# Kernel optimization log

Measured on AMD Instinct MI355X. Metric: run time of the kernel, lower is better.

Reference implementation:

```python
import jax, jax.numpy as jnp
import numpy as np

B, S, D = 4, 2048, 1024
H = 4 * D          # expert hidden dim
E_SPEC = 4         # num specific experts
E_SHR = 2          # num shared experts
TOP_K = 2


def setup_inputs() -> dict:
    key = jax.random.key(0)
    ks = jax.random.split(key, 16)
    s = 0.02
    return {
        "x": jax.random.normal(ks[0], (B, S, D), jnp.float32),
        # specific experts (stacked over expert axis)
        "spec_w1": jax.random.normal(ks[1], (E_SPEC, D, H), jnp.float32) * s,
        "spec_b1": jnp.zeros((E_SPEC, H), jnp.float32),
        "spec_w2": jax.random.normal(ks[2], (E_SPEC, H, D), jnp.float32) * s,
        "spec_b2": jnp.zeros((E_SPEC, D), jnp.float32),
        "spec_rw": jax.random.normal(ks[3], (D, E_SPEC), jnp.float32) * s,
        "spec_rb": jnp.zeros((E_SPEC,), jnp.float32),
        # shared experts
        "shr_w1": jax.random.normal(ks[4], (E_SHR, D, H), jnp.float32) * s,
        "shr_b1": jnp.zeros((E_SHR, H), jnp.float32),
        "shr_w2": jax.random.normal(ks[5], (E_SHR, H, D), jnp.float32) * s,
        "shr_b2": jnp.zeros((E_SHR, D), jnp.float32),
        "shr_rw": jax.random.normal(ks[6], (D, E_SHR), jnp.float32) * s,
        "shr_rb": jnp.zeros((E_SHR,), jnp.float32),
    }


def _expert_mlp(xf, w1, b1, w2, b2):
    # xf: [T, D]; w1: [E, D, H]; w2: [E, H, D] -> [E, T, D]
    h = jax.nn.gelu(jnp.einsum("td,edh->eth", xf, w1) + b1[:, None, :],
                    approximate=False)
    return jnp.einsum("eth,ehd->etd", h, w2) + b2[:, None, :]


def reference(x, spec_w1, spec_b1, spec_w2, spec_b2, spec_rw, spec_rb,
              shr_w1, shr_b1, shr_w2, shr_b2, shr_rw, shr_rb):
    b, s, d = x.shape
    xf = x.reshape(-1, d)                      # [T, D]
    T = xf.shape[0]

    # --- specific (top-k) routing ---
    spec_probs = jax.nn.softmax(xf @ spec_rw + spec_rb, axis=-1)   # [T, E]
    topk_probs, topk_idx = jax.lax.top_k(spec_probs, TOP_K)        # [T, K]

    # aux load-balancing loss
    counts = jnp.zeros((E_SPEC,), jnp.float32).at[topk_idx.reshape(-1)].add(1.0)
    fraction = counts / (T * TOP_K)
    aux_loss = E_SPEC * jnp.sum(fraction * spec_probs.mean(axis=0))

    # gate[t, e] = sum_k topk_probs[t,k] * 1[topk_idx[t,k]==e]
    gate = jnp.sum(jax.nn.one_hot(topk_idx, E_SPEC, dtype=xf.dtype)
                   * topk_probs[..., None], axis=1)                # [T, E]

    spec_out_e = _expert_mlp(xf, spec_w1, spec_b1, spec_w2, spec_b2)  # [E, T, D]
    specific_out = jnp.einsum("te,etd->td", gate, spec_out_e)

    # --- shared (dense) experts ---
    shr_probs = jax.nn.softmax(xf @ shr_rw + shr_rb, axis=-1)      # [T, E_shr]
    shr_out_e = _expert_mlp(xf, shr_w1, shr_b1, shr_w2, shr_b2)    # [E_shr, T, D]
    shared_out = jnp.einsum("te,etd->td", shr_probs, shr_out_e)

    final = (specific_out + shared_out).reshape(b, s, d)
    return final, aux_loss
```

## Files before the change

kernel.cpp:

```cpp
#include <hip/hip_runtime.h>
#include <hip/hip_bf16.h>

#define T_TOK 8192
#define DDIM 1024
#define HDIM 4096

typedef __bf16 bf16;
typedef bf16 bf16x8 __attribute__((ext_vector_type(8)));
typedef float f32x4 __attribute__((ext_vector_type(4)));

#define ASM_VMCNT(n) asm volatile("s_waitcnt vmcnt(" #n ")" ::: "memory")
#define MFMA16(a, b, c) __builtin_amdgcn_mfma_f32_16x16x32_bf16((a), (b), (c), 0, 0, 0)
#define G8_BAR __builtin_amdgcn_s_barrier()
#define G8_WAIT                                            \
  asm volatile("s_waitcnt lgkmcnt(0)" ::: "memory");       \
  __builtin_amdgcn_sched_barrier(0)

__device__ __forceinline__ void gl_lds16(const void* g, void* l) {
  __builtin_amdgcn_global_load_lds(
      (const __attribute__((address_space(1))) unsigned int*)g,
      (__attribute__((address_space(3))) unsigned int*)l, 16, 0, 0);
}

__device__ __forceinline__ float gelu_f(float v) {
  const float x = v * 0.7071067811865475f;
  const float ax = fabsf(x);
  const float t = 1.0f / fmaf(0.3275911f, ax, 1.0f);
  float p = fmaf(1.061405429f, t, -1.453152027f);
  p = fmaf(p, t, 1.421413741f);
  p = fmaf(p, t, -0.284496736f);
  p = fmaf(p, t, 0.254829592f);
  p = p * t;
  const float e = __expf(-ax * ax);
  const float er = fmaf(-p, e, 1.0f);
  const float erfx = (x >= 0.0f) ? er : -er;
  return 0.5f * v * (1.0f + erfx);
}

__global__ __launch_bounds__(256) void conv_router(
    const float* __restrict__ x, bf16* __restrict__ xb,
    const float* __restrict__ srw, const float* __restrict__ srb,
    const float* __restrict__ hrw, const float* __restrict__ hrb,
    float* __restrict__ gate, float4* __restrict__ probs4,
    int* __restrict__ top2) {
  const int lane = threadIdx.x & 63;
  const int w = threadIdx.x >> 6;
  const int t = blockIdx.x * 4 + w;

  const float* xr = x + (size_t)t * DDIM;
  bf16* xbr = xb + (size_t)t * DDIM;
  float p0 = 0, p1 = 0, p2 = 0, p3 = 0, p4 = 0, p5 = 0;
#pragma unroll
  for (int c = 0; c < 4; ++c) {
    const int d = c * 256 + lane * 4;
    const float4 xv = *(const float4*)(xr + d);
    bf16 ov[4] = {(bf16)xv.x, (bf16)xv.y, (bf16)xv.z, (bf16)xv.w};
    *(float2*)(xbr + d) = *(float2*)ov;
    const float xa[4] = {xv.x, xv.y, xv.z, xv.w};
#pragma unroll
    for (int j = 0; j < 4; ++j) {
      const float xd = xa[j];
      const float4 r4 = *(const float4*)(srw + (size_t)(d + j) * 4);
      p0 += xd * r4.x; p1 += xd * r4.y; p2 += xd * r4.z; p3 += xd * r4.w;
      const float2 r2 = *(const float2*)(hrw + (size_t)(d + j) * 2);
      p4 += xd * r2.x; p5 += xd * r2.y;
    }
  }
#pragma unroll
  for (int off = 32; off >= 1; off >>= 1) {
    p0 += __shfl_xor(p0, off);
    p1 += __shfl_xor(p1, off);
    p2 += __shfl_xor(p2, off);
    p3 += __shfl_xor(p3, off);
    p4 += __shfl_xor(p4, off);
    p5 += __shfl_xor(p5, off);
  }
  if (lane == 0) {
    const float l0 = p0 + srb[0], l1 = p1 + srb[1];
    const float l2 = p2 + srb[2], l3 = p3 + srb[3];
    const float m = fmaxf(fmaxf(l0, l1), fmaxf(l2, l3));
    const float e0 = expf(l0 - m), e1 = expf(l1 - m);
    const float e2 = expf(l2 - m), e3 = expf(l3 - m);
    const float s = e0 + e1 + e2 + e3;
    float pr[4] = {e0 / s, e1 / s, e2 / s, e3 / s};
    int i1 = 0; float v1 = pr[0];
#pragma unroll
    for (int e = 1; e < 4; ++e) if (pr[e] > v1) { v1 = pr[e]; i1 = e; }
    int i2 = -1; float v2 = -1.0f;
#pragma unroll
    for (int e = 0; e < 4; ++e)
      if (e != i1 && pr[e] > v2) { v2 = pr[e]; i2 = e; }
    float g[4] = {0, 0, 0, 0};
    g[i1] = v1; g[i2] = v2;
    float* gr = gate + (size_t)t * 8;
    gr[0] = g[0]; gr[1] = g[1]; gr[2] = g[2]; gr[3] = g[3];
    const float h0 = p4 + hrb[0], h1 = p5 + hrb[1];
    const float mh = fmaxf(h0, h1);
    const float q0 = expf(h0 - mh), q1 = expf(h1 - mh);
    const float qs = q0 + q1;
    gr[4] = q0 / qs; gr[5] = q1 / qs; gr[6] = 0; gr[7] = 0;
    probs4[t] = make_float4(pr[0], pr[1], pr[2], pr[3]);
    top2[t] = i1 | (i2 << 8);
  }
}

__global__ __launch_bounds__(256) void transpose_convert6(
    const float* __restrict__ spec_w, const float* __restrict__ shr_w,
    bf16* __restrict__ dst, int R, int C) {
  __shared__ float tile[32][33];
  const int z = blockIdx.z;
  const float* src = (z < 4) ? spec_w + (size_t)z * R * C
                             : shr_w + (size_t)(z - 4) * R * C;
  bf16* d = dst + (size_t)z * R * C;
  const int c0 = blockIdx.x * 32, r0 = blockIdx.y * 32;
  const int tx = threadIdx.x & 31, ty = threadIdx.x >> 5;
#pragma unroll
  for (int i = 0; i < 4; ++i)
    tile[ty + 8 * i][tx] = src[(size_t)(r0 + ty + 8 * i) * C + c0 + tx];
  __syncthreads();
#pragma unroll
  for (int i = 0; i < 4; ++i)
    d[(size_t)(c0 + ty + 8 * i) * R + r0 + tx] = (bf16)tile[tx][ty + 8 * i];
}

__global__ __launch_bounds__(1024) void scan_build(
    const int* __restrict__ top2, const float4* __restrict__ probs4,
    int* __restrict__ meta, int* __restrict__ lists,
    float* __restrict__ auxg) {
  __shared__ unsigned long long sc[1024];
  __shared__ float4 rp[512];
  const int tid = threadIdx.x;

  int ee[8];
  unsigned long long c = 0;
  float4 ps = make_float4(0.f, 0.f, 0.f, 0.f);
#pragma unroll
  for (int j = 0; j < 8; ++j) {
    const int t = tid * 8 + j;
    const int p = top2[t];
    ee[j] = p;
    const int a = p & 15, b = (p >> 8) & 15;
    c += (1ULL << (16 * a)) + (1ULL << (16 * b));
    const float4 pv = probs4[t];
    ps.x += pv.x; ps.y += pv.y; ps.z += pv.z; ps.w += pv.w;
  }
  sc[tid] = c;
  __syncthreads();
  for (int off = 1; off < 1024; off <<= 1) {
    const unsigned long long mine = sc[tid];
    const unsigned long long prev = (tid >= off) ? sc[tid - off] : 0ULL;
    __syncthreads();
    sc[tid] = mine + prev;
    __syncthreads();
  }
  const unsigned long long incl = sc[tid];
  const unsigned long long tot = sc[1023];
  const unsigned long long excl = incl - c;
  int q0 = (int)(excl & 0xffff), q1 = (int)((excl >> 16) & 0xffff);
  int q2 = (int)((excl >> 32) & 0xffff), q3 = (int)((excl >> 48) & 0xffff);
#pragma unroll
  for (int j = 0; j < 8; ++j) {
    const int t = tid * 8 + j;
    const int a = ee[j] & 15, b = (ee[j] >> 8) & 15;
    const int pa = (a == 0) ? q0 : (a == 1) ? q1 : (a == 2) ? q2 : q3;
    lists[a * 8192 + pa] = t;
    q0 += (a == 0); q1 += (a == 1); q2 += (a == 2); q3 += (a == 3);
    const int pb = (b == 0) ? q0 : (b == 1) ? q1 : (b == 2) ? q2 : q3;
    lists[b * 8192 + pb] = t;
    q0 += (b == 0); q1 += (b == 1); q2 += (b == 2); q3 += (b == 3);
  }
  if (tid == 1023) {
    const int c0 = (int)(tot & 0xffff), c1 = (int)((tot >> 16) & 0xffff);
    const int c2 = (int)((tot >> 32) & 0xffff), c3 = (int)((tot >> 48) & 0xffff);
    meta[24] = c0; meta[25] = c1; meta[26] = c2; meta[27] = c3;
    auxg[0] = (float)c0; auxg[1] = (float)c1;
    auxg[2] = (float)c2; auxg[3] = (float)c3;
    const int nb0 = (c0 + 255) >> 8, nb1 = (c1 + 255) >> 8;
    const int nb2 = (c2 + 255) >> 8, nb3 = (c3 + 255) >> 8;
    const int ch0 = (nb0 + 3) >> 2, ch1 = (nb1 + 3) >> 2;
    const int ch2 = (nb2 + 3) >> 2, ch3 = (nb3 + 3) >> 2;
    meta[34] = 0;
    meta[35] = nb0 * 256;
    meta[36] = meta[35] + nb1 * 256;
    meta[37] = meta[36] + nb2 * 256;
    meta[40] = 0;
    meta[41] = 64 * ch0;
    meta[42] = meta[41] + 64 * ch1;
    meta[43] = meta[42] + 64 * ch2;
    meta[44] = meta[43] + 64 * ch3;
  }
  if (tid >= 512) rp[tid - 512] = ps;
  __syncthreads();
  if (tid < 512) {
    const float4 o = rp[tid];
    ps.x += o.x; ps.y += o.y; ps.z += o.z; ps.w += o.w;
  }
  for (int w = 256; w >= 1; w >>= 1) {
    __syncthreads();
    if (tid >= w && tid < 2 * w) rp[tid - w] = ps;
    __syncthreads();
    if (tid < w) {
      const float4 o = rp[tid];
      ps.x += o.x; ps.y += o.y; ps.z += o.z; ps.w += o.w;
    }
  }
  if (tid == 0) {
    auxg[4] = ps.x; auxg[5] = ps.y; auxg[6] = ps.z; auxg[7] = ps.w;
  }
}

__global__ void aux_finalize(const float* __restrict__ auxg,
                             float* __restrict__ outp) {
  float a = 0.0f;
#pragma unroll
  for (int e = 0; e < 4; ++e)
    a += (auxg[e] / (float)(T_TOK * 2)) * (auxg[4 + e] / (float)T_TOK);
  outp[0] = 4.0f * a;
}

template <int KIND>
__global__ __launch_bounds__(512, 2) void g8(
    const bf16* __restrict__ A, const bf16* __restrict__ Bw,
    const float* __restrict__ bias, bf16* __restrict__ h_all, int N,
    int CH_M, int CH_N, const int* __restrict__ meta,
    const int* __restrict__ lists, int e) {
  __shared__ __align__(1024) bf16 Alds[2 * 256 * 64];
  __shared__ __align__(1024) bf16 Blds[2 * 256 * 64];

  const int tid = threadIdx.x;
  const int lane = tid & 63, wid = tid >> 6;
  const int wm = wid >> 2, wn = wid & 3;
  const int lr = lane & 15, lg = lane >> 4;

  int bm, bn, hb = 0, s = e;
  const bf16* Bp = Bw;
  const float* biasp = bias;
  if constexpr (KIND == 0) {
    const int xcd = blockIdx.x & 7, idx = blockIdx.x >> 3;
    bm = (xcd >> 1) * CH_M + idx / CH_N;
    bn = (xcd & 1) * CH_N + idx % CH_N;
  } else if constexpr (KIND == 1) {
    const int b = blockIdx.x;
    if (b >= meta[44]) return;
    s = (b >= meta[41]) + (b >= meta[42]) + (b >= meta[43]);
    const int local = b - meta[40 + s];
    const int nbm = (meta[24 + s] + 255) >> 8;
    const int CHm = (nbm + 3) >> 2;
    if (local >= 64 * CHm) return;
    const int xc = local & 7, idx = local >> 3;
    bm = (xc >> 1) * CHm + idx / 8;
    bn = (xc & 1) * 8 + idx % 8;
    if (bm >= nbm) return;
    hb = meta[34 + s];
    Bp = Bw + (size_t)s * DDIM * HDIM;
    biasp = bias + (size_t)s * HDIM;
  } else {
    const int nbm = (meta[24 + e] + 255) >> 8;
    const int CHm = (nbm + 3) >> 2;
    if (blockIdx.x >= 64 * CHm) return;
    const int xc = blockIdx.x & 7, idx = blockIdx.x >> 3;
    bm = (xc >> 1) * CHm + idx / 8;
    bn = (xc & 1) * 8 + idx % 8;
    if (bm >= nbm) return;
  }
  const int K = DDIM;
  const int NT = K >> 6;

  const int rl = tid >> 3;
  const int cbs = ((tid * 16) & 127) ^ ((rl & 7) << 4);
  int ar[4];
#pragma unroll
  for (int c = 0; c < 4; ++c) ar[c] = bm * 256 + c * 64 + rl;
  if constexpr (KIND != 0) {
    const int* lp = lists + s * 8192;
#pragma unroll
    for (int c = 0; c < 4; ++c) {
      const int t = lp[ar[c]];
      ar[c] = t < 0 ? 0 : t;
    }
  }
  const bf16* sA[4];
  const bf16* sB[4];
#pragma unroll
  for (int c = 0; c < 4; ++c) {
    sA[c] = A + (size_t)ar[c] * K + (cbs >> 1);
    sB[c] = Bp + (size_t)(bn * 256 + c * 64 + rl) * K + (cbs >> 1);
  }
  char* const ldsA = (char*)Alds;
  char* const ldsB = (char*)Blds;
  const int wb = wid * 1024;

  const int ax0 = (lg * 16) ^ ((lr & 7) << 4);
  const int ax1 = ax0 ^ 64;
  const int aro = (wm * 128 + lr) * 128;
  const int bro = (wn * 64 + lr) * 128;
  const char* const A0 = (const char*)Alds + aro + ax0;
  const char* const A1 = (const char*)Alds + aro + ax1;
  const char* const B0 = (const char*)Blds + bro + ax0;
  const char* const B1 = (const char*)Blds + bro + ax1;

  f32x4 acc[8][4] = {};
  bf16x8 af[4][2], b01[2][2], b23[2][2];

#define G8_RA(BOFF, MB)                                               \
  _Pragma("unroll") for (int i = 0; i < 4; ++i) {                     \
    af[i][0] = *(const bf16x8*)(A0 + (BOFF) + ((MB) + i) * 2048);     \
    af[i][1] = *(const bf16x8*)(A1 + (BOFF) + ((MB) + i) * 2048);     \
  }
#define G8_RB(BOFF, DST, NB)                                          \
  _Pragma("unroll") for (int i = 0; i < 2; ++i) {                     \
    DST[i][0] = *(const bf16x8*)(B0 + (BOFF) + ((NB) + i) * 2048);    \
    DST[i][1] = *(const bf16x8*)(B1 + (BOFF) + ((NB) + i) * 2048);    \
  }
#define G8_MMA(MB, NB, BSRC)                                          \
  __builtin_amdgcn_s_setprio(1);                                      \
  _Pragma("unroll") for (int i = 0; i < 4; ++i)                       \
    _Pragma("unroll") for (int j = 0; j < 2; ++j) {                   \
      acc[(MB) + i][(NB) + j] =                                       \
          MFMA16(af[i][0], BSRC[j][0], acc[(MB) + i][(NB) + j]);      \
      acc[(MB) + i][(NB) + j] =                                       \
          MFMA16(af[i][1], BSRC[j][1], acc[(MB) + i][(NB) + j]);      \
    }                                                                 \
  __builtin_amdgcn_s_setprio(0);
#define G8_STG_B(T, C, BUFO)                                          \
  gl_lds16(sB[C] + (size_t)(T) * 64, ldsB + (BUFO) + (C) * 8192 + wb);
#define G8_STG_A(T, C, BUFO)                                          \
  gl_lds16(sA[C] + (size_t)(T) * 64, ldsA + (BUFO) + (C) * 8192 + wb);

  G8_STG_B(0, 0, 0) G8_STG_B(0, 1, 0) G8_STG_B(0, 2, 0) G8_STG_B(0, 3, 0)
  G8_STG_A(0, 0, 0) G8_STG_A(0, 1, 0) G8_STG_A(0, 2, 0) G8_STG_A(0, 3, 0)
  G8_STG_B(1, 0, 32768) G8_STG_B(1, 1, 32768)
  G8_STG_B(1, 2, 32768) G8_STG_B(1, 3, 32768)
  G8_STG_A(1, 0, 32768) G8_STG_A(1, 1, 32768)
  G8_STG_A(1, 2, 32768) G8_STG_A(1, 3, 32768)
  ASM_VMCNT(8);
  G8_BAR;

  for (int t = 0; t < NT; t += 2) {
    const bool stg = (t + 2) < NT;
    G8_RA(0, 0);
    G8_RB(0, b01, 0);
    G8_BAR; G8_WAIT;
    G8_MMA(0, 0, b01);
    G8_BAR;
    G8_RB(0, b23, 2);
    G8_BAR; G8_WAIT;
    G8_MMA(0, 2, b23);
    G8_BAR;
    G8_RA(0, 4);
    if (stg) { G8_STG_B(t + 2, 0, 0) G8_STG_B(t + 2, 1, 0) }
    G8_BAR; G8_WAIT;
    G8_MMA(4, 0, b01);
    G8_BAR;
    if (stg) { G8_STG_B(t + 2, 2, 0) G8_STG_B(t + 2, 3, 0) }
    G8_MMA(4, 2, b23);
    if (stg) ASM_VMCNT(4); else ASM_VMCNT(0);
    G8_BAR;
    G8_RA(32768, 0);
    G8_RB(32768, b01, 0);
    if (stg) { G8_STG_A(t + 2, 0, 0) G8_STG_A(t + 2, 1, 0) }
    G8_BAR; G8_WAIT;
    G8_MMA(0, 0, b01);
    G8_BAR;
    G8_RB(32768, b23, 2);
    if (stg) { G8_STG_A(t + 2, 2, 0) G8_STG_A(t + 2, 3, 0) }
    G8_BAR; G8_WAIT;
    G8_MMA(0, 2, b23);
    G8_BAR;
    G8_RA(32768, 4);
    if (stg) {
      G8_STG_B(t + 3, 0, 32768) G8_STG_B(t + 3, 1, 32768)
      G8_STG_B(t + 3, 2, 32768) G8_STG_B(t + 3, 3, 32768)
    }
    G8_BAR; G8_WAIT;
    G8_MMA(4, 0, b01);
    G8_BAR;
    if (stg) {
      G8_STG_A(t + 3, 0, 32768) G8_STG_A(t + 3, 1, 32768)
      G8_STG_A(t + 3, 2, 32768) G8_STG_A(t + 3, 3, 32768)
    }
    G8_MMA(4, 2, b23);
    if (stg) ASM_VMCNT(8);
    G8_BAR;
  }

  const int colb = bn * 256 + wn * 64;
  const int rowb = hb + bm * 256 + wm * 128 + lg * 4;
  float bv[4];
#pragma unroll
  for (int nf = 0; nf < 4; ++nf) bv[nf] = biasp[colb + nf * 16 + lr];
#pragma unroll
  for (int mf = 0; mf < 8; ++mf)
#pragma unroll
    for (int nf = 0; nf < 4; ++nf) {
      const int col = colb + nf * 16 + lr;
#pragma unroll
      for (int r = 0; r < 4; ++r) {
        const int row = rowb + mf * 16 + r;
        h_all[(size_t)row * N + col] = (bf16)gelu_f(acc[mf][nf][r] + bv[nf]);
      }
    }
}

template <int EMODE>
__global__ __launch_bounds__(512, 2) void g2k(
    const bf16* __restrict__ A, int lda, const bf16* __restrict__ B,
    const float* __restrict__ bias, float* __restrict__ out,
    const float* __restrict__ gate, int gidx, const int* __restrict__ meta,
    const int* __restrict__ lists, int e, int packed) {
  __shared__ __align__(1024) bf16 Alds[2 * 256 * 64];
  __shared__ __align__(1024) bf16 Blds[2 * 128 * 64];

  const int tid = threadIdx.x;
  const int lane = tid & 63, wid = tid >> 6;
  const int wm = wid >> 2, wn = wid & 3;
  const int lr = lane & 15, lg = lane >> 4;

  int bm, bn, hb = 0;
  if constexpr (EMODE == 3) {
    const int nbm = (meta[24 + e] + 255) >> 8;
    const int CHm = (nbm + 3) >> 2;
    if (blockIdx.x >= 8 * CHm * 4) return;
    const int xc = blockIdx.x & 7, idx = blockIdx.x >> 3;
    bm = (xc >> 1) * CHm + idx / 4;
    bn = (xc & 1) * 4 + idx % 4;
    if (bm >= nbm) return;
    hb = packed ? meta[34 + e] : 0;
  } else {
    const int xcd = blockIdx.x & 7, idx = blockIdx.x >> 3;
    bm = (xcd >> 1) * 8 + idx / 4;
    bn = (xcd & 1) * 4 + idx % 4;
  }
  const int K = HDIM, N = DDIM;
  const int NT = K >> 6;

  const int L = tid * 16;
  const int rl = L >> 7;
  const int colb = (L & 127) ^ ((rl & 7) << 4);

  const int ar0 = hb + bm * 256 + rl;
  const bf16* sAc0 = A + (size_t)ar0 * lda + (colb >> 1);
  const bf16* sAc1 = A + (size_t)(ar0 + 64) * lda + (colb >> 1);
  const bf16* sAc2 = A + (size_t)(ar0 + 128) * lda + (colb >> 1);
  const bf16* sAc3 = A + (size_t)(ar0 + 192) * lda + (colb >> 1);
  const bf16* sB = B + (size_t)(bn * 128 + rl) * K + (colb >> 1);

  char* const ldsA = (char*)Alds;
  char* const ldsB = (char*)Blds;
  const int wb = wid * 1024;
  char* const stA[2] = {ldsA + wb, ldsA + 32768 + wb};
  char* const stB[2] = {ldsB + wb, ldsB + 16384 + wb};

  const int ax0 = (lg * 16) ^ ((lr & 7) << 4);
  const int ax1 = ax0 ^ 64;
  const int aro = (wm * 128 + lr) * 128;
  const int bro = (wn * 32 + lr) * 128;
  const char* const Ak0[2] = {ldsA + aro + ax0, ldsA + 32768 + aro + ax0};
  const char* const Ak1[2] = {ldsA + aro + ax1, ldsA + 32768 + aro + ax1};
  const char* const Bk0[2] = {ldsB + bro + ax0, ldsB + 16384 + bro + ax0};
  const char* const Bk1[2] = {ldsB + bro + ax1, ldsB + 16384 + bro + ax1};

  f32x4 acc[8][2] = {};

  gl_lds16(sAc0, stA[0]);
  gl_lds16(sAc1, stA[0] + 8192);
  gl_lds16(sAc2, stA[0] + 16384);
  gl_lds16(sAc3, stA[0] + 24576);
  gl_lds16(sB, stB[0]);
  gl_lds16(sB + (size_t)64 * K, stB[0] + 8192);
  gl_lds16(sB + 64, stB[1]);
  gl_lds16(sB + (size_t)64 * K + 64, stB[1] + 8192);
  gl_lds16(sAc0 + 64, stA[1]);
  gl_lds16(sAc1 + 64, stA[1] + 8192);
  ASM_VMCNT(4);
  __builtin_amdgcn_s_barrier();

  for (int kt0 = 0; kt0 < NT; kt0 += 2) {
#pragma unroll
    for (int par = 0; par < 2; ++par) {
      const int kt = kt0 + par;
      const int cur = par, oth = par ^ 1;
      const bool st1 = (kt + 1) < NT, st2 = (kt + 2) < NT;
      const size_t ko1 = (size_t)(kt + 1) << 6, ko2 = (size_t)(kt + 2) << 6;
      const char* Ac0 = Ak0[cur]; const char* Ac1 = Ak1[cur];
      const char* Bc0 = Bk0[cur]; const char* Bc1 = Bk1[cur];

      bf16x8 af[4][2], bfr[2][2];

#pragma unroll
      for (int mf = 0; mf < 4; ++mf) {
        af[mf][0] = *(const bf16x8*)(Ac0 + mf * 2048);
        af[mf][1] = *(const bf16x8*)(Ac1 + mf * 2048);
      }
      bfr[0][0] = *(const bf16x8*)(Bc0);
      bfr[0][1] = *(const bf16x8*)(Bc1);
      if (st1) {
        gl_lds16(sAc2 + ko1, stA[oth] + 16384);
        gl_lds16(sAc3 + ko1, stA[oth] + 24576);
      }
      __builtin_amdgcn_s_barrier();
      asm volatile("s_waitcnt lgkmcnt(0)" ::: "memory");
      __builtin_amdgcn_sched_barrier(0);
      __builtin_amdgcn_s_setprio(1);
#pragma unroll
      for (int mf = 0; mf < 4; ++mf) {
        acc[mf][0] = MFMA16(af[mf][0], bfr[0][0], acc[mf][0]);
        acc[mf][0] = MFMA16(af[mf][1], bfr[0][1], acc[mf][0]);
      }
      __builtin_amdgcn_s_setprio(0);
      __builtin_amdgcn_s_barrier();

      bfr[1][0] = *(const bf16x8*)(Bc0 + 2048);
      bfr[1][1] = *(const bf16x8*)(Bc1 + 2048);
      __builtin_amdgcn_s_barrier();
      asm volatile("s_waitcnt lgkmcnt(0)" ::: "memory");
      __builtin_amdgcn_sched_barrier(0);
      __builtin_amdgcn_s_setprio(1);
#pragma unroll
      for (int mf = 0; mf < 4; ++mf) {
        acc[mf][1] = MFMA16(af[mf][0], bfr[1][0], acc[mf][1]);
        acc[mf][1] = MFMA16(af[mf][1], bfr[1][1], acc[mf][1]);
      }
      __builtin_amdgcn_s_setprio(0);
      __builtin_amdgcn_s_barrier();

#pragma unroll
      for (int mf = 0; mf < 4; ++mf) {
        af[mf][0] = *(const bf16x8*)(Ac0 + 8192 + mf * 2048);
        af[mf][1] = *(const bf16x8*)(Ac1 + 8192 + mf * 2048);
      }
      if (st2) {
        gl_lds16(sB + ko2, stB[cur]);
        gl_lds16(sB + (size_t)64 * K + ko2, stB[cur] + 8192);
      }
      __builtin_amdgcn_s_barrier();
      asm volatile("s_waitcnt lgkmcnt(0)" ::: "memory");
      __builtin_amdgcn_sched_barrier(0);
      __builtin_amdgcn_s_setprio(1);
#pragma unroll
      for (int mf = 0; mf < 4; ++mf) {
        acc[4 + mf][0] = MFMA16(af[mf][0], bfr[0][0], acc[4 + mf][0]);
        acc[4 + mf][0] = MFMA16(af[mf][1], bfr[0][1], acc[4 + mf][0]);
      }
      __builtin_amdgcn_s_setprio(0);
      __builtin_amdgcn_s_barrier();

      if (st2) {
        gl_lds16(sAc0 + ko2, stA[cur]);
        gl_lds16(sAc1 + ko2, stA[cur] + 8192);
      }
      __builtin_amdgcn_s_setprio(1);
#pragma unroll
      for (int mf = 0; mf < 4; ++mf) {
        acc[4 + mf][1] = MFMA16(af[mf][0], bfr[1][0], acc[4 + mf][1]);
        acc[4 + mf][1] = MFMA16(af[mf][1], bfr[1][1], acc[4 + mf][1]);
      }
      __builtin_amdgcn_s_setprio(0);
      if (st2) {
        ASM_VMCNT(4);
        __builtin_amdgcn_s_barrier();
      } else if (st1) {
        ASM_VMCNT(0);
        __builtin_amdgcn_s_barrier();
      }
    }
  }

  const int colb2 = bn * 128 + wn * 32;
  const int rowb = bm * 256 + wm * 128 + lg * 4;
  float bv[2];
#pragma unroll
  for (int nf = 0; nf < 2; ++nf) bv[nf] = bias[colb2 + nf * 16 + lr];
#pragma unroll
  for (int mf = 0; mf < 8; ++mf) {
    if constexpr (EMODE != 3) {
      float gv[4];
#pragma unroll
      for (int r = 0; r < 4; ++r)
        gv[r] = gate[(size_t)(rowb + mf * 16 + r) * 8 + gidx];
#pragma unroll
      for (int nf = 0; nf < 2; ++nf) {
        const int col = colb2 + nf * 16 + lr;
#pragma unroll
        for (int r = 0; r < 4; ++r) {
          const float v = acc[mf][nf][r] + bv[nf];
          const size_t oi = (size_t)(rowb + mf * 16 + r) * N + col;
          if constexpr (EMODE == 1)
            out[oi] += gv[r] * v;
          else
            out[oi] = gv[r] * v;
        }
      }
    } else {
      const int* lp = lists + e * 8192;
      int tok[4]; float gv[4];
#pragma unroll
      for (int r = 0; r < 4; ++r) {
        tok[r] = lp[rowb + mf * 16 + r];
        gv[r] = tok[r] >= 0 ? gate[(size_t)tok[r] * 8 + gidx] : 0.0f;
      }
#pragma unroll
      for (int nf = 0; nf < 2; ++nf) {
        const int col = colb2 + nf * 16 + lr;
#pragma unroll
        for (int r = 0; r < 4; ++r) {
          if (tok[r] >= 0) {
            const float v = acc[mf][nf][r] + bv[nf];
            out[(size_t)tok[r] * N + col] += gv[r] * v;
          }
        }
      }
    }
  }
}

extern "C" void kernel_launch(void* const* d_in, const int* in_sizes, int n_in,
                              void* d_out, int out_size, void* d_ws,
                              size_t ws_size, hipStream_t stream) {
  const float* x = (const float*)d_in[0];
  const float* spec_w1 = (const float*)d_in[1];
  const float* spec_b1 = (const float*)d_in[2];
  const float* spec_w2 = (const float*)d_in[3];
  const float* spec_b2 = (const float*)d_in[4];
  const float* spec_rw = (const float*)d_in[5];
  const float* spec_rb = (const float*)d_in[6];
  const float* shr_w1 = (const float*)d_in[7];
  const float* shr_b1 = (const float*)d_in[8];
  const float* shr_w2 = (const float*)d_in[9];
  const float* shr_b2 = (const float*)d_in[10];
  const float* shr_rw = (const float*)d_in[11];
  const float* shr_rb = (const float*)d_in[12];
  float* out = (float*)d_out;

  char* ws = (char*)d_ws;
  const size_t DH = (size_t)DDIM * HDIM;
  const size_t OFF_W1 = 16777216;
  const size_t OFF_W2 = OFF_W1 + 50331648;
  const size_t OFF_GATE = OFF_W2 + 50331648;
  const size_t OFF_AUX = OFF_GATE + 262144;
  const size_t OFF_META = OFF_AUX + 256;
  const size_t OFF_LIST = OFF_META + 256;
  const size_t OFF_T2 = OFF_LIST + 131072;
  const size_t OFF_P4 = OFF_T2 + 32768;
  const size_t OFF_H = OFF_P4 + 131072 + 1024;
  bf16* xb = (bf16*)ws;
  bf16* w1t = (bf16*)(ws + OFF_W1);
  bf16* w2t = (bf16*)(ws + OFF_W2);
  float* gate = (float*)(ws + OFF_GATE);
  float* auxg = (float*)(ws + OFF_AUX);
  int* meta = (int*)(ws + OFF_META);
  int* lists = (int*)(ws + OFF_LIST);
  int* top2 = (int*)(ws + OFF_T2);
  float4* probs4 = (float4*)(ws + OFF_P4);
  bf16* h = (bf16*)(ws + OFF_H);

  const bool rich = ws_size >= OFF_H + (size_t)17408 * HDIM * 2;

  hipMemsetAsync(lists, 0xFF, 4 * 8192 * 4, stream);

  conv_router<<<T_TOK / 4, 256, 0, stream>>>(x, xb, spec_rw, spec_rb, shr_rw,
                                             shr_rb, gate, probs4, top2);
  scan_build<<<1, 1024, 0, stream>>>(top2, probs4, meta, lists, auxg);

  transpose_convert6<<<dim3(HDIM / 32, DDIM / 32, 6), 256, 0, stream>>>(
      spec_w1, shr_w1, w1t, DDIM, HDIM);
  transpose_convert6<<<dim3(DDIM / 32, HDIM / 32, 6), 256, 0, stream>>>(
      spec_w2, shr_w2, w2t, HDIM, DDIM);

  if (rich) {
    g8<0><<<1024, 512, 0, stream>>>(xb, w1t + 4 * DH, shr_b1, h, 8192,
                                    8, 16, meta, lists, 0);
    g2k<0><<<256, 512, 0, stream>>>(h, 8192, w2t + 4 * DH, shr_b2, out,
                                    gate, 4, meta, lists, 0, 0);
    g2k<1><<<256, 512, 0, stream>>>(h + 4096, 8192, w2t + 5 * DH,
                                    shr_b2 + 1024, out, gate, 5, meta,
                                    lists, 0, 0);
    g8<1><<<2048, 512, 0, stream>>>(xb, w1t, spec_b1, h, 4096,
                                    0, 8, meta, lists, 0);
    for (int e = 0; e < 4; ++e)
      g2k<3><<<256, 512, 0, stream>>>(h, 4096, w2t + (size_t)e * DH,
                                      spec_b2 + (size_t)e * DDIM, out, gate,
                                      e, meta, lists, e, 1);
  } else {
    for (int es = 0; es < 2; ++es) {
      g8<0><<<512, 512, 0, stream>>>(xb, w1t + (4 + es) * DH,
                                     shr_b1 + (size_t)es * HDIM, h, 4096,
                                     8, 8, meta, lists, 0);
      if (es == 0)
        g2k<0><<<256, 512, 0, stream>>>(h, 4096, w2t + 4 * DH, shr_b2, out,
                                        gate, 4, meta, lists, 0, 0);
      else
        g2k<1><<<256, 512, 0, stream>>>(h, 4096, w2t + 5 * DH,
                                        shr_b2 + 1024, out, gate, 5, meta,
                                        lists, 0, 0);
    }
    for (int e = 0; e < 4; ++e) {
      g8<2><<<512, 512, 0, stream>>>(xb, w1t + (size_t)e * DH,
                                     spec_b1 + (size_t)e * HDIM, h, 4096,
                                     0, 8, meta, lists, e);
      g2k<3><<<256, 512, 0, stream>>>(h, 4096, w2t + (size_t)e * DH,
                                      spec_b2 + (size_t)e * DDIM, out, gate,
                                      e, meta, lists, e, 0);
    }
  }
  aux_finalize<<<1, 1, 0, stream>>>(auxg, out + (size_t)T_TOK * DDIM);
}
```

Measured before the change: 1.016 ms.

## Fold gates into hidden activations and batch the down-projections across experts

Each token's routing gate is now multiplied into the GELU output of the first GEMM. The second-stage GEMMs can then sum expert contributions directly, with the bias scaled by the gate. The two shared experts become one K=8192 GEMM that writes the output once instead of read-modify-writing it. The four specific-expert down-projections become a single launch that writes packed bf16 partials, and a small per-token kernel gathers each token's two partials and adds them to the output. This removes several launches and most float read-modify-write traffic on the output, at the cost of an extra bf16 partial buffer, an extra reduction pass, and bf16 rounding of gated activations and partials.

```diff
diff --git a/kernel.cpp b/kernel.cpp
--- a/kernel.cpp
+++ b/kernel.cpp
@@ -125,7 +125,7 @@
 
 __global__ __launch_bounds__(1024) void scan_build(
     const int* __restrict__ top2, const float4* __restrict__ probs4,
-    int* __restrict__ meta, int* __restrict__ lists,
+    int* __restrict__ meta, int* __restrict__ lists, int2* __restrict__ tpos,
     float* __restrict__ auxg) {
   __shared__ unsigned long long sc[1024];
   __shared__ float4 rp[512];
@@ -168,6 +168,7 @@
     const int pb = (b == 0) ? q0 : (b == 1) ? q1 : (b == 2) ? q2 : q3;
     lists[b * 8192 + pb] = t;
     q0 += (b == 0); q1 += (b == 1); q2 += (b == 2); q3 += (b == 3);
+    tpos[t] = make_int2(a * 8192 + pa, b * 8192 + pb);
   }
   if (tid == 1023) {
     const int c0 = (int)(tot & 0xffff), c1 = (int)((tot >> 16) & 0xffff);
@@ -188,6 +189,11 @@
     meta[42] = meta[41] + 64 * ch1;
     meta[43] = meta[42] + 64 * ch2;
     meta[44] = meta[43] + 64 * ch3;
+    meta[46] = 0;
+    meta[47] = 32 * ch0;
+    meta[48] = meta[47] + 32 * ch1;
+    meta[49] = meta[48] + 32 * ch2;
+    meta[50] = meta[49] + 32 * ch3;
   }
   if (tid >= 512) rp[tid - 512] = ps;
   __syncthreads();
@@ -223,7 +229,7 @@
     const bf16* __restrict__ A, const bf16* __restrict__ Bw,
     const float* __restrict__ bias, bf16* __restrict__ h_all, int N,
     int CH_M, int CH_N, const int* __restrict__ meta,
-    const int* __restrict__ lists, int e) {
+    const int* __restrict__ lists, const float* __restrict__ gate) {
   __shared__ __align__(1024) bf16 Alds[2 * 256 * 64];
   __shared__ __align__(1024) bf16 Blds[2 * 256 * 64];
 
@@ -232,14 +238,14 @@
   const int wm = wid >> 2, wn = wid & 3;
   const int lr = lane & 15, lg = lane >> 4;
 
-  int bm, bn, hb = 0, s = e;
+  int bm, bn, hb = 0, s = 0;
   const bf16* Bp = Bw;
   const float* biasp = bias;
   if constexpr (KIND == 0) {
     const int xcd = blockIdx.x & 7, idx = blockIdx.x >> 3;
     bm = (xcd >> 1) * CH_M + idx / CH_N;
     bn = (xcd & 1) * CH_N + idx % CH_N;
-  } else if constexpr (KIND == 1) {
+  } else {
     const int b = blockIdx.x;
     if (b >= meta[44]) return;
     s = (b >= meta[41]) + (b >= meta[42]) + (b >= meta[43]);
@@ -254,14 +260,6 @@
     hb = meta[34 + s];
     Bp = Bw + (size_t)s * DDIM * HDIM;
     biasp = bias + (size_t)s * HDIM;
-  } else {
-    const int nbm = (meta[24 + e] + 255) >> 8;
-    const int CHm = (nbm + 3) >> 2;
-    if (blockIdx.x >= 64 * CHm) return;
-    const int xc = blockIdx.x & 7, idx = blockIdx.x >> 3;
-    bm = (xc >> 1) * CHm + idx / 8;
-    bn = (xc & 1) * 8 + idx % 8;
-    if (bm >= nbm) return;
   }
   const int K = DDIM;
   const int NT = K >> 6;
@@ -385,29 +383,41 @@
   }
 
   const int colb = bn * 256 + wn * 64;
-  const int rowb = hb + bm * 256 + wm * 128 + lg * 4;
+  const int rowb = bm * 256 + wm * 128 + lg * 4;
   float bv[4];
 #pragma unroll
   for (int nf = 0; nf < 4; ++nf) bv[nf] = biasp[colb + nf * 16 + lr];
-#pragma unroll
-  for (int mf = 0; mf < 8; ++mf)
+  const int sgid = (KIND == 0) ? 4 + (bn >> 4) : s;
+#pragma unroll
+  for (int mf = 0; mf < 8; ++mf) {
+    float gv[4];
+#pragma unroll
+    for (int r = 0; r < 4; ++r) {
+      const int lrow = rowb + mf * 16 + r;
+      if constexpr (KIND == 0) {
+        gv[r] = gate[(size_t)lrow * 8 + sgid];
+      } else {
+        const int tok = lists[s * 8192 + lrow];
+        gv[r] = tok >= 0 ? gate[(size_t)tok * 8 + sgid] : 0.0f;
+      }
+    }
 #pragma unroll
     for (int nf = 0; nf < 4; ++nf) {
       const int col = colb + nf * 16 + lr;
 #pragma unroll
       for (int r = 0; r < 4; ++r) {
-        const int row = rowb + mf * 16 + r;
-        h_all[(size_t)row * N + col] = (bf16)gelu_f(acc[mf][nf][r] + bv[nf]);
-      }
-    }
-}
-
-template <int EMODE>
-__global__ __launch_bounds__(512, 2) void g2k(
-    const bf16* __restrict__ A, int lda, const bf16* __restrict__ B,
-    const float* __restrict__ bias, float* __restrict__ out,
-    const float* __restrict__ gate, int gidx, const int* __restrict__ meta,
-    const int* __restrict__ lists, int e, int packed) {
+        const int row = hb + rowb + mf * 16 + r;
+        h_all[(size_t)row * N + col] =
+            (bf16)(gv[r] * gelu_f(acc[mf][nf][r] + bv[nf]));
+      }
+    }
+  }
+}
+
+__global__ __launch_bounds__(512, 2) void g2sh(
+    const bf16* __restrict__ A, const bf16* __restrict__ w2_0,
+    const bf16* __restrict__ w2_1, const float* __restrict__ b2,
+    float* __restrict__ out, const float* __restrict__ gate) {
   __shared__ __align__(1024) bf16 Alds[2 * 256 * 64];
   __shared__ __align__(1024) bf16 Blds[2 * 128 * 64];
 
@@ -416,8 +426,208 @@
   const int wm = wid >> 2, wn = wid & 3;
   const int lr = lane & 15, lg = lane >> 4;
 
-  int bm, bn, hb = 0;
-  if constexpr (EMODE == 3) {
+  const int xcd = blockIdx.x & 7, idx = blockIdx.x >> 3;
+  const int bm = (xcd >> 1) * 8 + idx / 4;
+  const int bn = (xcd & 1) * 4 + idx % 4;
+  const int lda = 8192, N = DDIM;
+  const int NT = 128;
+
+  const int L = tid * 16;
+  const int rl = L >> 7;
+  const int colb = (L & 127) ^ ((rl & 7) << 4);
+
+  const int ar0 = bm * 256 + rl;
+  const bf16* sAc0 = A + (size_t)ar0 * lda + (colb >> 1);
+  const bf16* sAc1 = A + (size_t)(ar0 + 64) * lda + (colb >> 1);
+  const bf16* sAc2 = A + (size_t)(ar0 + 128) * lda + (colb >> 1);
+  const bf16* sAc3 = A + (size_t)(ar0 + 192) * lda + (colb >> 1);
+  const bf16* pB[2][2];
+  pB[0][0] = w2_0 + (size_t)(bn * 128 + rl) * 4096 + (colb >> 1);
+  pB[0][1] = w2_0 + (size_t)(bn * 128 + 64 + rl) * 4096 + (colb >> 1);
+  pB[1][0] = w2_1 + (size_t)(bn * 128 + rl) * 4096 + (colb >> 1);
+  pB[1][1] = w2_1 + (size_t)(bn * 128 + 64 + rl) * 4096 + (colb >> 1);
+
+  char* const ldsA = (char*)Alds;
+  char* const ldsB = (char*)Blds;
+  const int wb = wid * 1024;
+  char* const stA[2] = {ldsA + wb, ldsA + 32768 + wb};
+  char* const stB[2] = {ldsB + wb, ldsB + 16384 + wb};
+
+  const int ax0 = (lg * 16) ^ ((lr & 7) << 4);
+  const int ax1 = ax0 ^ 64;
+  const int aro = (wm * 128 + lr) * 128;
+  const int bro = (wn * 32 + lr) * 128;
+  const char* const Ak0[2] = {ldsA + aro + ax0, ldsA + 32768 + aro + ax0};
+  const char* const Ak1[2] = {ldsA + aro + ax1, ldsA + 32768 + aro + ax1};
+  const char* const Bk0[2] = {ldsB + bro + ax0, ldsB + 16384 + bro + ax0};
+  const char* const Bk1[2] = {ldsB + bro + ax1, ldsB + 16384 + bro + ax1};
+
+  f32x4 acc[8][2] = {};
+
+#define G2S_STB(T, DST)                                                   \
+  {                                                                       \
+    const int hh = (T) >> 6;                                              \
+    const size_t oo = (size_t)((T) & 63) * 64;                            \
+    gl_lds16(pB[hh][0] + oo, DST);                                        \
+    gl_lds16(pB[hh][1] + oo, DST + 8192);                                 \
+  }
+
+  gl_lds16(sAc0, stA[0]);
+  gl_lds16(sAc1, stA[0] + 8192);
+  gl_lds16(sAc2, stA[0] + 16384);
+  gl_lds16(sAc3, stA[0] + 24576);
+  G2S_STB(0, stB[0])
+  G2S_STB(1, stB[1])
+  gl_lds16(sAc0 + 64, stA[1]);
+  gl_lds16(sAc1 + 64, stA[1] + 8192);
+  ASM_VMCNT(4);
+  __builtin_amdgcn_s_barrier();
+
+  for (int kt0 = 0; kt0 < NT; kt0 += 2) {
+#pragma unroll
+    for (int par = 0; par < 2; ++par) {
+      const int kt = kt0 + par;
+      const int cur = par, oth = par ^ 1;
+      const bool st1 = (kt + 1) < NT, st2 = (kt + 2) < NT;
+      const size_t ko1 = (size_t)(kt + 1) << 6, ko2 = (size_t)(kt + 2) << 6;
+      const char* Ac0 = Ak0[cur]; const char* Ac1 = Ak1[cur];
+      const char* Bc0 = Bk0[cur]; const char* Bc1 = Bk1[cur];
+
+      bf16x8 af[4][2], bfr[2][2];
+
+#pragma unroll
+      for (int mf = 0; mf < 4; ++mf) {
+        af[mf][0] = *(const bf16x8*)(Ac0 + mf * 2048);
+        af[mf][1] = *(const bf16x8*)(Ac1 + mf * 2048);
+      }
+      bfr[0][0] = *(const bf16x8*)(Bc0);
+      bfr[0][1] = *(const bf16x8*)(Bc1);
+      if (st1) {
+        gl_lds16(sAc2 + ko1, stA[oth] + 16384);
+        gl_lds16(sAc3 + ko1, stA[oth] + 24576);
+      }
+      __builtin_amdgcn_s_barrier();
+      asm volatile("s_waitcnt lgkmcnt(0)" ::: "memory");
+      __builtin_amdgcn_sched_barrier(0);
+      __builtin_amdgcn_s_setprio(1);
+#pragma unroll
+      for (int mf = 0; mf < 4; ++mf) {
+        acc[mf][0] = MFMA16(af[mf][0], bfr[0][0], acc[mf][0]);
+        acc[mf][0] = MFMA16(af[mf][1], bfr[0][1], acc[mf][0]);
+      }
+      __builtin_amdgcn_s_setprio(0);
+      __builtin_amdgcn_s_barrier();
+
+      bfr[1][0] = *(const bf16x8*)(Bc0 + 2048);
+      bfr[1][1] = *(const bf16x8*)(Bc1 + 2048);
+      __builtin_amdgcn_s_barrier();
+      asm volatile("s_waitcnt lgkmcnt(0)" ::: "memory");
+      __builtin_amdgcn_sched_barrier(0);
+      __builtin_amdgcn_s_setprio(1);
+#pragma unroll
+      for (int mf = 0; mf < 4; ++mf) {
+        acc[mf][1] = MFMA16(af[mf][0], bfr[1][0], acc[mf][1]);
+        acc[mf][1] = MFMA16(af[mf][1], bfr[1][1], acc[mf][1]);
+      }
+      __builtin_amdgcn_s_setprio(0);
+      __builtin_amdgcn_s_barrier();
+
+#pragma unroll
+      for (int mf = 0; mf < 4; ++mf) {
+        af[mf][0] = *(const bf16x8*)(Ac0 + 8192 + mf * 2048);
+        af[mf][1] = *(const bf16x8*)(Ac1 + 8192 + mf * 2048);
+      }
+      if (st2) G2S_STB(kt + 2, stB[cur])
+      __builtin_amdgcn_s_barrier();
+      asm volatile("s_waitcnt lgkmcnt(0)" ::: "memory");
+      __builtin_amdgcn_sched_barrier(0);
+      __builtin_amdgcn_s_setprio(1);
+#pragma unroll
+      for (int mf = 0; mf < 4; ++mf) {
+        acc[4 + mf][0] = MFMA16(af[mf][0], bfr[0][0], acc[4 + mf][0]);
+        acc[4 + mf][0] = MFMA16(af[mf][1], bfr[0][1], acc[4 + mf][0]);
+      }
+      __builtin_amdgcn_s_setprio(0);
+      __builtin_amdgcn_s_barrier();
+
+      if (st2) {
+        gl_lds16(sAc0 + ko2, stA[cur]);
+        gl_lds16(sAc1 + ko2, stA[cur] + 8192);
+      }
+      __builtin_amdgcn_s_setprio(1);
+#pragma unroll
+      for (int mf = 0; mf < 4; ++mf) {
+        acc[4 + mf][1] = MFMA16(af[mf][0], bfr[1][0], acc[4 + mf][1]);
+        acc[4 + mf][1] = MFMA16(af[mf][1], bfr[1][1], acc[4 + mf][1]);
+      }
+      __builtin_amdgcn_s_setprio(0);
+      if (st2) {
+        ASM_VMCNT(4);
+        __builtin_amdgcn_s_barrier();
+      } else if (st1) {
+        ASM_VMCNT(0);
+        __builtin_amdgcn_s_barrier();
+      }
+    }
+  }
+
+  const int colb2 = bn * 128 + wn * 32;
+  const int rowb = bm * 256 + wm * 128 + lg * 4;
+  float bv0[2], bv1[2];
+#pragma unroll
+  for (int nf = 0; nf < 2; ++nf) {
+    bv0[nf] = b2[colb2 + nf * 16 + lr];
+    bv1[nf] = b2[1024 + colb2 + nf * 16 + lr];
+  }
+#pragma unroll
+  for (int mf = 0; mf < 8; ++mf) {
+    float g4[4], g5[4];
+#pragma unroll
+    for (int r = 0; r < 4; ++r) {
+      const size_t row = rowb + mf * 16 + r;
+      g4[r] = gate[row * 8 + 4];
+      g5[r] = gate[row * 8 + 5];
+    }
+#pragma unroll
+    for (int nf = 0; nf < 2; ++nf) {
+      const int col = colb2 + nf * 16 + lr;
+#pragma unroll
+      for (int r = 0; r < 4; ++r) {
+        out[(size_t)(rowb + mf * 16 + r) * N + col] =
+            acc[mf][nf][r] + g4[r] * bv0[nf] + g5[r] * bv1[nf];
+      }
+    }
+  }
+}
+
+template <int PMODE>
+__global__ __launch_bounds__(512, 2) void g2sp(
+    const bf16* __restrict__ h_all, const bf16* __restrict__ w2t,
+    const float* __restrict__ spec_b2, float* __restrict__ out,
+    bf16* __restrict__ P, const float* __restrict__ gate,
+    const int* __restrict__ meta, const int* __restrict__ lists, int e) {
+  __shared__ __align__(1024) bf16 Alds[2 * 256 * 64];
+  __shared__ __align__(1024) bf16 Blds[2 * 128 * 64];
+
+  const int tid = threadIdx.x;
+  const int lane = tid & 63, wid = tid >> 6;
+  const int wm = wid >> 2, wn = wid & 3;
+  const int lr = lane & 15, lg = lane >> 4;
+
+  int bm, bn, s = e;
+  if constexpr (PMODE == 1) {
+    const int b = blockIdx.x;
+    if (b >= meta[50]) return;
+    s = (b >= meta[47]) + (b >= meta[48]) + (b >= meta[49]);
+    const int local = b - meta[46 + s];
+    const int nbm = (meta[24 + s] + 255) >> 8;
+    const int CHm = (nbm + 3) >> 2;
+    if (local >= 32 * CHm) return;
+    const int xc = local & 7, idx = local >> 3;
+    bm = (xc >> 1) * CHm + idx / 4;
+    bn = (xc & 1) * 4 + idx % 4;
+    if (bm >= nbm) return;
+  } else {
     const int nbm = (meta[24 + e] + 255) >> 8;
     const int CHm = (nbm + 3) >> 2;
     if (blockIdx.x >= 8 * CHm * 4) return;
@@ -425,12 +635,10 @@
     bm = (xc >> 1) * CHm + idx / 4;
     bn = (xc & 1) * 4 + idx % 4;
     if (bm >= nbm) return;
-    hb = packed ? meta[34 + e] : 0;
-  } else {
-    const int xcd = blockIdx.x & 7, idx = blockIdx.x >> 3;
-    bm = (xcd >> 1) * 8 + idx / 4;
-    bn = (xcd & 1) * 4 + idx % 4;
-  }
+  }
+  const int hb = meta[34 + s];
+  const bf16* B = w2t + (size_t)s * DDIM * HDIM;
+  const float* bias = spec_b2 + (size_t)s * DDIM;
   const int K = HDIM, N = DDIM;
   const int NT = K >> 6;
 
@@ -439,10 +647,10 @@
   const int colb = (L & 127) ^ ((rl & 7) << 4);
 
   const int ar0 = hb + bm * 256 + rl;
-  const bf16* sAc0 = A + (size_t)ar0 * lda + (colb >> 1);
-  const bf16* sAc1 = A + (size_t)(ar0 + 64) * lda + (colb >> 1);
-  const bf16* sAc2 = A + (size_t)(ar0 + 128) * lda + (colb >> 1);
-  const bf16* sAc3 = A + (size_t)(ar0 + 192) * lda + (colb >> 1);
+  const bf16* sAc0 = h_all + (size_t)ar0 * K + (colb >> 1);
+  const bf16* sAc1 = h_all + (size_t)(ar0 + 64) * K + (colb >> 1);
+  const bf16* sAc2 = h_all + (size_t)(ar0 + 128) * K + (colb >> 1);
+  const bf16* sAc3 = h_all + (size_t)(ar0 + 192) * K + (colb >> 1);
   const bf16* sB = B + (size_t)(bn * 128 + rl) * K + (colb >> 1);
 
   char* const ldsA = (char*)Alds;
@@ -571,47 +779,51 @@
   float bv[2];
 #pragma unroll
   for (int nf = 0; nf < 2; ++nf) bv[nf] = bias[colb2 + nf * 16 + lr];
+  const int* lp = lists + s * 8192;
 #pragma unroll
   for (int mf = 0; mf < 8; ++mf) {
-    if constexpr (EMODE != 3) {
-      float gv[4];
-#pragma unroll
-      for (int r = 0; r < 4; ++r)
-        gv[r] = gate[(size_t)(rowb + mf * 16 + r) * 8 + gidx];
-#pragma unroll
-      for (int nf = 0; nf < 2; ++nf) {
-        const int col = colb2 + nf * 16 + lr;
-#pragma unroll
-        for (int r = 0; r < 4; ++r) {
-          const float v = acc[mf][nf][r] + bv[nf];
-          const size_t oi = (size_t)(rowb + mf * 16 + r) * N + col;
-          if constexpr (EMODE == 1)
-            out[oi] += gv[r] * v;
-          else
-            out[oi] = gv[r] * v;
+    int tok[4]; float gv[4];
+#pragma unroll
+    for (int r = 0; r < 4; ++r) {
+      tok[r] = lp[rowb + mf * 16 + r];
+      gv[r] = tok[r] >= 0 ? gate[(size_t)tok[r] * 8 + s] : 0.0f;
+    }
+#pragma unroll
+    for (int nf = 0; nf < 2; ++nf) {
+      const int col = colb2 + nf * 16 + lr;
+#pragma unroll
+      for (int r = 0; r < 4; ++r) {
+        const float v = acc[mf][nf][r] + gv[r] * bv[nf];
+        if constexpr (PMODE == 1) {
+          P[(size_t)(hb + rowb + mf * 16 + r) * N + col] = (bf16)v;
+        } else {
+          if (tok[r] >= 0) out[(size_t)tok[r] * N + col] += v;
         }
       }
-    } else {
-      const int* lp = lists + e * 8192;
-      int tok[4]; float gv[4];
-#pragma unroll
-      for (int r = 0; r < 4; ++r) {
-        tok[r] = lp[rowb + mf * 16 + r];
-        gv[r] = tok[r] >= 0 ? gate[(size_t)tok[r] * 8 + gidx] : 0.0f;
-      }
-#pragma unroll
-      for (int nf = 0; nf < 2; ++nf) {
-        const int col = colb2 + nf * 16 + lr;
-#pragma unroll
-        for (int r = 0; r < 4; ++r) {
-          if (tok[r] >= 0) {
-            const float v = acc[mf][nf][r] + bv[nf];
-            out[(size_t)tok[r] * N + col] += gv[r] * v;
-          }
-        }
-      }
-    }
-  }
+    }
+  }
+}
+
+__global__ __launch_bounds__(256) void reduce_spec(
+    const bf16* __restrict__ P, const int2* __restrict__ tpos,
+    const int* __restrict__ meta, float* __restrict__ out) {
+  const int t = blockIdx.x;
+  const int c = threadIdx.x * 4;
+  const int2 tp = tpos[t];
+  const int ea = tp.x >> 13, pa = tp.x & 8191;
+  const int eb = tp.y >> 13, pb = tp.y & 8191;
+  const size_t ra = (size_t)(meta[34 + ea] + pa) * DDIM + c;
+  const size_t rb = (size_t)(meta[34 + eb] + pb) * DDIM + c;
+  const bf16x8* pav = (const bf16x8*)&P[ra];
+  float4 o = *(float4*)&out[(size_t)t * DDIM + c];
+  const bf16* A4 = &P[ra];
+  const bf16* B4 = &P[rb];
+  o.x += (float)A4[0] + (float)B4[0];
+  o.y += (float)A4[1] + (float)B4[1];
+  o.z += (float)A4[2] + (float)B4[2];
+  o.w += (float)A4[3] + (float)B4[3];
+  (void)pav;
+  *(float4*)&out[(size_t)t * DDIM + c] = o;
 }
 
 extern "C" void kernel_launch(void* const* d_in, const int* in_sizes, int n_in,
@@ -642,7 +854,11 @@
   const size_t OFF_LIST = OFF_META + 256;
   const size_t OFF_T2 = OFF_LIST + 131072;
   const size_t OFF_P4 = OFF_T2 + 32768;
-  const size_t OFF_H = OFF_P4 + 131072 + 1024;
+  const size_t OFF_TPOS = OFF_P4 + 131072 + 1024;
+  const size_t OFF_H = OFF_TPOS + 65536;
+  const size_t H_BYTES = (size_t)17408 * HDIM * 2;
+  const size_t OFF_P = OFF_H + H_BYTES;
+  const size_t P_BYTES = (size_t)17408 * DDIM * 2;
   bf16* xb = (bf16*)ws;
   bf16* w1t = (bf16*)(ws + OFF_W1);
   bf16* w2t = (bf16*)(ws + OFF_W2);
@@ -652,56 +868,37 @@
   int* lists = (int*)(ws + OFF_LIST);
   int* top2 = (int*)(ws + OFF_T2);
   float4* probs4 = (float4*)(ws + OFF_P4);
+  int2* tpos = (int2*)(ws + OFF_TPOS);
   bf16* h = (bf16*)(ws + OFF_H);
-
-  const bool rich = ws_size >= OFF_H + (size_t)17408 * HDIM * 2;
+  bf16* P = (bf16*)(ws + OFF_P);
+
+  const bool ppath = ws_size >= OFF_P + P_BYTES;
 
   hipMemsetAsync(lists, 0xFF, 4 * 8192 * 4, stream);
 
   conv_router<<<T_TOK / 4, 256, 0, stream>>>(x, xb, spec_rw, spec_rb, shr_rw,
                                              shr_rb, gate, probs4, top2);
-  scan_build<<<1, 1024, 0, stream>>>(top2, probs4, meta, lists, auxg);
+  scan_build<<<1, 1024, 0, stream>>>(top2, probs4, meta, lists, tpos, auxg);
 
   transpose_convert6<<<dim3(HDIM / 32, DDIM / 32, 6), 256, 0, stream>>>(
       spec_w1, shr_w1, w1t, DDIM, HDIM);
   transpose_convert6<<<dim3(DDIM / 32, HDIM / 32, 6), 256, 0, stream>>>(
       spec_w2, shr_w2, w2t, HDIM, DDIM);
 
-  if (rich) {
-    g8<0><<<1024, 512, 0, stream>>>(xb, w1t + 4 * DH, shr_b1, h, 8192,
-                                    8, 16, meta, lists, 0);
-    g2k<0><<<256, 512, 0, stream>>>(h, 8192, w2t + 4 * DH, shr_b2, out,
-                                    gate, 4, meta, lists, 0, 0);
-    g2k<1><<<256, 512, 0, stream>>>(h + 4096, 8192, w2t + 5 * DH,
-                                    shr_b2 + 1024, out, gate, 5, meta,
-                                    lists, 0, 0);
-    g8<1><<<2048, 512, 0, stream>>>(xb, w1t, spec_b1, h, 4096,
-                                    0, 8, meta, lists, 0);
+  g8<0><<<1024, 512, 0, stream>>>(xb, w1t + 4 * DH, shr_b1, h, 8192,
+                                  8, 16, meta, lists, gate);
+  g2sh<<<256, 512, 0, stream>>>(h, w2t + 4 * DH, w2t + 5 * DH, shr_b2, out,
+                                gate);
+  g8<1><<<2048, 512, 0, stream>>>(xb, w1t, spec_b1, h, 4096,
+                                  0, 8, meta, lists, gate);
+  if (ppath) {
+    g2sp<1><<<1024, 512, 0, stream>>>(h, w2t, spec_b2, out, P, gate, meta,
+                                      lists, 0);
+    reduce_spec<<<T_TOK, 256, 0, stream>>>(P, tpos, meta, out);
+  } else {
     for (int e = 0; e < 4; ++e)
-      g2k<3><<<256, 512, 0, stream>>>(h, 4096, w2t + (size_t)e * DH,
-                                      spec_b2 + (size_t)e * DDIM, out, gate,
-                                      e, meta, lists, e, 1);
-  } else {
-    for (int es = 0; es < 2; ++es) {
-      g8<0><<<512, 512, 0, stream>>>(xb, w1t + (4 + es) * DH,
-                                     shr_b1 + (size_t)es * HDIM, h, 4096,
-                                     8, 8, meta, lists, 0);
-      if (es == 0)
-        g2k<0><<<256, 512, 0, stream>>>(h, 4096, w2t + 4 * DH, shr_b2, out,
-                                        gate, 4, meta, lists, 0, 0);
-      else
-        g2k<1><<<256, 512, 0, stream>>>(h, 4096, w2t + 5 * DH,
-                                        shr_b2 + 1024, out, gate, 5, meta,
-                                        lists, 0, 0);
-    }
-    for (int e = 0; e < 4; ++e) {
-      g8<2><<<512, 512, 0, stream>>>(xb, w1t + (size_t)e * DH,
-                                     spec_b1 + (size_t)e * HDIM, h, 4096,
-                                     0, 8, meta, lists, e);
-      g2k<3><<<256, 512, 0, stream>>>(h, 4096, w2t + (size_t)e * DH,
-                                      spec_b2 + (size_t)e * DDIM, out, gate,
-                                      e, meta, lists, e, 0);
-    }
+      g2sp<0><<<256, 512, 0, stream>>>(h, w2t, spec_b2, out, nullptr, gate,
+                                       meta, lists, e);
   }
   aux_finalize<<<1, 1, 0, stream>>>(auxg, out + (size_t)T_TOK * DDIM);
 }
```

After: 1.062 ms. 4.6% more time.
